# Kernel tuning notes

Hardware: AMD Instinct MI355X
Metric: run time of the kernel (lower is better)

## Reference

```python
import jax, jax.numpy as jnp
import numpy as np

NUM_TRUE = 8
NUM_NULL = 2
NUM_EXPERTS = NUM_TRUE + NUM_NULL
TOP_K = 2


def setup_inputs() -> dict:
    key = jax.random.key(0)
    k0, k1, k2 = jax.random.split(key, 3)
    B, S, D = 4, 2048, 1024
    inputs = jax.random.normal(k0, (B, S, D), dtype=jnp.float32)
    gate_w = jax.random.normal(k1, (NUM_EXPERTS, D), dtype=jnp.float32) * 0.02
    gate_b = jnp.zeros((NUM_EXPERTS,), dtype=jnp.float32)
    # expert_w stored as [E, D_in, D_out] so expert i computes x @ expert_w[i] + expert_b[i]
    expert_w = jax.random.normal(k2, (NUM_TRUE, D, D), dtype=jnp.float32) * 0.02
    expert_b = jnp.zeros((NUM_TRUE, D), dtype=jnp.float32)
    return {"inputs": inputs, "gate_w": gate_w, "gate_b": gate_b,
            "expert_w": expert_w, "expert_b": expert_b}


def reference(inputs, gate_w, gate_b, expert_w, expert_b):
    D = inputs.shape[-1]
    x = inputs.reshape(-1, D)                       # [T, D]
    gate_logits = x @ gate_w.T + gate_b             # [T, E]
    gate_probs = jax.nn.softmax(gate_logits, axis=-1)
    weights, selected = jax.lax.top_k(gate_probs, TOP_K)  # [T, K]
    true_mask = selected < NUM_TRUE                 # null experts contribute nothing
    true_weights = weights * true_mask
    denom = true_weights.sum(axis=-1, keepdims=True)
    denom = jnp.where(denom > 0, denom, jnp.ones_like(denom))
    norm_w = (true_weights / denom).astype(x.dtype)  # [T, K]
    # per-(token, true-expert) combine weight; zero for unselected experts
    one_hot = jax.nn.one_hot(selected, NUM_EXPERTS, dtype=norm_w.dtype)  # [T, K, E]
    combine_w = jnp.einsum('tk,tke->te', norm_w, one_hot)[:, :NUM_TRUE]  # [T, E_true]
    # dense expert evaluation, then weighted combine (zero weights cancel
    # exactly as the gather/scatter loop in the torch code)
    expert_out = jnp.einsum('td,edh->teh', x, expert_w) + expert_b[None, :, :]  # [T, E_true, D]
    out = jnp.einsum('te,teh->th', combine_w, expert_out)  # [T, D]
    return out.reshape(inputs.shape[:-1] + (out.shape[-1],))
```

## Files before the change

kernel.cpp:

```cpp
#include <hip/hip_runtime.h>
#include <hip/hip_bf16.h>
#include <stdint.h>

#define T_TOKENS 8192
#define D_DIM    1024
#define NE       10
#define NT       8

typedef unsigned short u16;
typedef __attribute__((ext_vector_type(8))) __bf16 bf16x8;
typedef __attribute__((ext_vector_type(4))) float  f32x4;

__device__ __forceinline__ u16 f32_to_bf16(float f) {
  union { float f; uint32_t u; } v; v.f = f;
  uint32_t u = v.u;
  return (u16)((u + 0x7fffu + ((u >> 16) & 1u)) >> 16);
}

__device__ __forceinline__ void async_load16(const u16* g, u16* l) {
  __builtin_amdgcn_global_load_lds(
      (const __attribute__((address_space(1))) void*)(const void*)g,
      (__attribute__((address_space(3))) void*)(void*)l, 16, 0, 0);
}

__global__ __launch_bounds__(256) void gate_kernel(
    const float* __restrict__ x, const float* __restrict__ gw,
    const float* __restrict__ gb, u16* __restrict__ xb,
    int* __restrict__ cnt, int* __restrict__ tokList, float* __restrict__ wList) {
  __shared__ float gws[NE * D_DIM];
  __shared__ float gbs[NE];
  __shared__ int   se[32];
  __shared__ float swt[32];
  int tid = threadIdx.x;
  for (int i = tid; i < NE * D_DIM; i += 256) gws[i] = gw[i];
  if (tid < NE) gbs[tid] = gb[tid];
  __syncthreads();
  int lane = tid & 63;
  int wv   = tid >> 6;
  for (int it = 0; it < 4; ++it) {
    int slot = wv * 4 + it;
    int t = blockIdx.x * 16 + slot;
    const float* xr = x + (size_t)t * D_DIM;
    float xv[16];
#pragma unroll
    for (int j = 0; j < 16; ++j) xv[j] = xr[lane + 64 * j];
#pragma unroll
    for (int j = 0; j < 16; ++j)
      xb[(size_t)t * D_DIM + lane + 64 * j] = f32_to_bf16(xv[j]);
    float logit[NE];
#pragma unroll
    for (int e = 0; e < NE; ++e) {
      float a = 0.f;
#pragma unroll
      for (int j = 0; j < 16; ++j)
        a = fmaf(xv[j], gws[e * D_DIM + lane + 64 * j], a);
#pragma unroll
      for (int off = 32; off >= 1; off >>= 1) a += __shfl_xor(a, off);
      logit[e] = a + gbs[e];
    }
    float mx = logit[0];
#pragma unroll
    for (int e = 1; e < NE; ++e) mx = fmaxf(mx, logit[e]);
    float p[NE]; float s = 0.f;
#pragma unroll
    for (int e = 0; e < NE; ++e) { p[e] = expf(logit[e] - mx); s += p[e]; }
    int e0 = 0; float b0 = p[0];
#pragma unroll
    for (int e = 1; e < NE; ++e) if (p[e] > b0) { b0 = p[e]; e0 = e; }
    int e1 = -1; float b1 = -1.f;
#pragma unroll
    for (int e = 0; e < NE; ++e) if (e != e0 && p[e] > b1) { b1 = p[e]; e1 = e; }
    float w0 = b0 / s, w1 = b1 / s;
    float tw0 = (e0 < NT) ? w0 : 0.f;
    float tw1 = (e1 < NT) ? w1 : 0.f;
    float denom = tw0 + tw1;
    float nw0 = 0.f, nw1 = 0.f;
    if (denom > 0.f) { nw0 = tw0 / denom; nw1 = tw1 / denom; }
    if (lane == 0) {
      se[slot * 2]      = (e0 < NT) ? e0 : -1;  swt[slot * 2]      = nw0;
      se[slot * 2 + 1]  = (e1 < NT) ? e1 : -1;  swt[slot * 2 + 1]  = nw1;
    }
  }
  __syncthreads();
  if (tid < NT * 2) {
    int e = tid >> 1, sl = tid & 1, c = 0;
    for (int i = sl; i < 32; i += 2) c += (se[i] == e);
    if (c > 0) {
      int seg = e * 2 + sl;
      int base = atomicAdd(&cnt[seg * 32], c);
      int j = 0;
      for (int i = sl; i < 32; i += 2) {
        if (se[i] == e) {
          tokList[seg * T_TOKENS + base + j] = blockIdx.x * 16 + (i >> 1);
          wList[seg * T_TOKENS + base + j]   = swt[i];
          ++j;
        }
      }
    }
  }
}

__global__ __launch_bounds__(256) void transpose_w(
    const float* __restrict__ W, u16* __restrict__ wT) {
  __shared__ float tile[64][65];
  int e  = blockIdx.z;
  int k0 = blockIdx.y * 64;
  int n0 = blockIdx.x * 64;
  int c  = threadIdx.x & 63;
  int r0 = threadIdx.x >> 6;
  const float* We = W + ((size_t)e << 20);
#pragma unroll
  for (int rr = 0; rr < 16; ++rr) {
    int r = rr * 4 + r0;
    tile[c][r] = We[(size_t)(k0 + r) * 1024 + n0 + c];
  }
  __syncthreads();
  u16* wTe = wT + ((size_t)e << 20);
#pragma unroll
  for (int rr = 0; rr < 16; ++rr) {
    int n = rr * 4 + r0;
    wTe[(size_t)(n0 + n) * 1024 + k0 + c] = f32_to_bf16(tile[n][c]);
  }
}

__global__ __launch_bounds__(256) void moe_gemm(
    const u16* __restrict__ xb, const u16* __restrict__ wT,
    const int* __restrict__ cnt, const int* __restrict__ tokList,
    const float* __restrict__ wList, const float* __restrict__ eb,
    float* __restrict__ out, int slot, int accum) {
  int e   = blockIdx.z;
  int seg = e * 2 + slot;
  int c   = cnt[seg * 32];
  int m0  = blockIdx.y * 128;
  if (m0 >= c) return;
  int n0  = blockIdx.x * 128;
  __shared__ __align__(16) u16 As[128 * 32];
  __shared__ __align__(16) u16 Bs[128 * 32];
  __shared__ int   tokS[128];
  __shared__ float wS[128];
  int tid = threadIdx.x;
  if (tid < 128) {
    int gm = m0 + tid;
    bool v = gm < c;
    tokS[tid] = v ? tokList[seg * T_TOKENS + gm] : 0;
    wS[tid]   = v ? wList[seg * T_TOKENS + gm]  : 0.f;
  }
  __syncthreads();
  int lane = tid & 63;
  int wv   = tid >> 6;
  int rl   = lane >> 2;
  int kcp  = lane & 3;
  int kcd  = kcp ^ (rl & 3);
  int rowL0 = wv * 32 + rl, rowL1 = rowL0 + 16;
  const u16* gA0 = xb + (size_t)tokS[rowL0] * 1024 + kcd * 8;
  const u16* gA1 = xb + (size_t)tokS[rowL1] * 1024 + kcd * 8;
  const u16* wTe = wT + ((size_t)e << 20);
  const u16* gB0 = wTe + (size_t)(n0 + rowL0) * 1024 + kcd * 8;
  const u16* gB1 = wTe + (size_t)(n0 + rowL1) * 1024 + kcd * 8;
  u16* lA0 = As + (wv * 32) * 32;
  u16* lA1 = As + (wv * 32 + 16) * 32;
  u16* lB0 = Bs + (wv * 32) * 32;
  u16* lB1 = Bs + (wv * 32 + 16) * 32;

  int wm = wv >> 1, wn = wv & 1;
  int lrow = lane & 15;
  int q    = lane >> 4;
  int sw   = (q ^ (lrow & 3)) * 8;
  f32x4 acc[4][4];
#pragma unroll
  for (int i = 0; i < 4; ++i)
#pragma unroll
    for (int j = 0; j < 4; ++j) acc[i][j] = (f32x4){0.f, 0.f, 0.f, 0.f};

  for (int k0 = 0; k0 < 1024; k0 += 32) {
    __syncthreads();
    async_load16(gA0 + k0, lA0);
    async_load16(gA1 + k0, lA1);
    async_load16(gB0 + k0, lB0);
    async_load16(gB1 + k0, lB1);
    __syncthreads();
    bf16x8 af[4], bfr[4];
#pragma unroll
    for (int mt = 0; mt < 4; ++mt)
      af[mt] = *(const bf16x8*)(As + (wm * 64 + mt * 16 + lrow) * 32 + sw);
#pragma unroll
    for (int nt = 0; nt < 4; ++nt)
      bfr[nt] = *(const bf16x8*)(Bs + (wn * 64 + nt * 16 + lrow) * 32 + sw);
#pragma unroll
    for (int mt = 0; mt < 4; ++mt)
#pragma unroll
      for (int nt = 0; nt < 4; ++nt)
        acc[mt][nt] = __builtin_amdgcn_mfma_f32_16x16x32_bf16(
            af[mt], bfr[nt], acc[mt][nt], 0, 0, 0);
  }
  int rq = lane >> 4;
  float bias[4];
#pragma unroll
  for (int nt = 0; nt < 4; ++nt)
    bias[nt] = eb[e * 1024 + n0 + wn * 64 + nt * 16 + lrow];
#pragma unroll
  for (int mt = 0; mt < 4; ++mt) {
#pragma unroll
    for (int r = 0; r < 4; ++r) {
      int ml = wm * 64 + mt * 16 + rq * 4 + r;
      if (m0 + ml < c) {
        int   t = tokS[ml];
        float w = wS[ml];
        float* orow = out + (size_t)t * 1024 + n0 + wn * 64 + lrow;
        if (accum) {
#pragma unroll
          for (int nt = 0; nt < 4; ++nt)
            orow[nt * 16] += w * (acc[mt][nt][r] + bias[nt]);
        } else {
#pragma unroll
          for (int nt = 0; nt < 4; ++nt)
            orow[nt * 16] = w * (acc[mt][nt][r] + bias[nt]);
        }
      }
    }
  }
}

extern "C" void kernel_launch(void* const* d_in, const int* in_sizes, int n_in,
                              void* d_out, int out_size, void* d_ws, size_t ws_size,
                              hipStream_t stream) {
  const float* x  = (const float*)d_in[0];
  const float* gw = (const float*)d_in[1];
  const float* gb = (const float*)d_in[2];
  const float* ew = (const float*)d_in[3];
  const float* eb = (const float*)d_in[4];
  float* out = (float*)d_out;
  char* ws = (char*)d_ws;
  int*   cnt     = (int*)ws;
  int*   tokList = (int*)(ws + 2048);
  float* wList   = (float*)(ws + 2048 + 16 * T_TOKENS * 4);
  u16*   xb      = (u16*)(ws + 2048 + 2 * 16 * T_TOKENS * 4);
  u16*   wT      = (u16*)(ws + 2048 + 2 * 16 * T_TOKENS * 4 + (size_t)T_TOKENS * D_DIM * 2);

  hipMemsetAsync(cnt, 0, 2048, stream);
  hipMemsetAsync(d_out, 0, (size_t)out_size * sizeof(float), stream);
  gate_kernel<<<512, 256, 0, stream>>>(x, gw, gb, xb, cnt, tokList, wList);
  transpose_w<<<dim3(16, 16, 8), 256, 0, stream>>>(ew, wT);
  moe_gemm<<<dim3(8, 24, 8), 256, 0, stream>>>(xb, wT, cnt, tokList, wList, eb, out, 0, 0);
  moe_gemm<<<dim3(8, 24, 8), 256, 0, stream>>>(xb, wT, cnt, tokList, wList, eb, out, 1, 1);
}
```

Baseline: 212.2 us.

## Merge MoE GEMM slots per expert, write bf16 outputs, add gather combine kernel

```diff
diff --git a/kernel.cpp b/kernel.cpp
--- a/kernel.cpp
+++ b/kernel.cpp
@@ -6,18 +6,24 @@
 #define D_DIM    1024
 #define NE       10
 #define NT       8
+#define SEG      2048
 
 typedef unsigned short u16;
 typedef __attribute__((ext_vector_type(8))) __bf16 bf16x8;
 typedef __attribute__((ext_vector_type(4))) float  f32x4;
-
-__device__ __forceinline__ u16 f32_to_bf16(float f) {
+typedef __attribute__((ext_vector_type(8))) unsigned short u16x8;
+typedef __attribute__((ext_vector_type(4))) unsigned short u16x4;
+
+static __device__ __forceinline__ u16 f32_to_bf16(float f) {
   union { float f; uint32_t u; } v; v.f = f;
   uint32_t u = v.u;
   return (u16)((u + 0x7fffu + ((u >> 16) & 1u)) >> 16);
 }
-
-__device__ __forceinline__ void async_load16(const u16* g, u16* l) {
+static __device__ __forceinline__ float bf16_to_f32(u16 u) {
+  union { uint32_t u; float f; } v; v.u = ((uint32_t)u) << 16; return v.f;
+}
+
+static __device__ __forceinline__ void async_load16(const u16* g, u16* l) {
   __builtin_amdgcn_global_load_lds(
       (const __attribute__((address_space(1))) void*)(const void*)g,
       (__attribute__((address_space(3))) void*)(void*)l, 16, 0, 0);
@@ -26,34 +32,48 @@
 __global__ __launch_bounds__(256) void gate_kernel(
     const float* __restrict__ x, const float* __restrict__ gw,
     const float* __restrict__ gb, u16* __restrict__ xb,
-    int* __restrict__ cnt, int* __restrict__ tokList, float* __restrict__ wList) {
+    int* __restrict__ cnt, int* __restrict__ tokList,
+    int* __restrict__ revIdx, float* __restrict__ revW) {
   __shared__ float gws[NE * D_DIM];
   __shared__ float gbs[NE];
   __shared__ int   se[32];
   __shared__ float swt[32];
   int tid = threadIdx.x;
-  for (int i = tid; i < NE * D_DIM; i += 256) gws[i] = gw[i];
+  {
+    const f32x4* g4 = (const f32x4*)gw;
+    f32x4* s4 = (f32x4*)gws;
+    for (int i = tid; i < NE * D_DIM / 4; i += 256) s4[i] = g4[i];
+  }
   if (tid < NE) gbs[tid] = gb[tid];
   __syncthreads();
   int lane = tid & 63;
   int wv   = tid >> 6;
+  const f32x4* gws4 = (const f32x4*)gws;
   for (int it = 0; it < 4; ++it) {
     int slot = wv * 4 + it;
     int t = blockIdx.x * 16 + slot;
-    const float* xr = x + (size_t)t * D_DIM;
-    float xv[16];
-#pragma unroll
-    for (int j = 0; j < 16; ++j) xv[j] = xr[lane + 64 * j];
-#pragma unroll
-    for (int j = 0; j < 16; ++j)
-      xb[(size_t)t * D_DIM + lane + 64 * j] = f32_to_bf16(xv[j]);
+    const f32x4* xr4 = (const f32x4*)(x + (size_t)t * D_DIM);
+    f32x4 xv[4];
+#pragma unroll
+    for (int jj = 0; jj < 4; ++jj) xv[jj] = xr4[lane + 64 * jj];
+    u16x4* xbr = (u16x4*)(xb + (size_t)t * D_DIM);
+#pragma unroll
+    for (int jj = 0; jj < 4; ++jj) {
+      u16x4 pk;
+#pragma unroll
+      for (int k = 0; k < 4; ++k) pk[k] = f32_to_bf16(xv[jj][k]);
+      xbr[lane + 64 * jj] = pk;
+    }
     float logit[NE];
 #pragma unroll
     for (int e = 0; e < NE; ++e) {
       float a = 0.f;
 #pragma unroll
-      for (int j = 0; j < 16; ++j)
-        a = fmaf(xv[j], gws[e * D_DIM + lane + 64 * j], a);
+      for (int jj = 0; jj < 4; ++jj) {
+        f32x4 gv = gws4[e * 256 + lane + 64 * jj];
+#pragma unroll
+        for (int k = 0; k < 4; ++k) a = fmaf(xv[jj][k], gv[k], a);
+      }
 #pragma unroll
       for (int off = 32; off >= 1; off >>= 1) a += __shfl_xor(a, off);
       logit[e] = a + gbs[e];
@@ -77,22 +97,26 @@
     float nw0 = 0.f, nw1 = 0.f;
     if (denom > 0.f) { nw0 = tw0 / denom; nw1 = tw1 / denom; }
     if (lane == 0) {
-      se[slot * 2]      = (e0 < NT) ? e0 : -1;  swt[slot * 2]      = nw0;
-      se[slot * 2 + 1]  = (e1 < NT) ? e1 : -1;  swt[slot * 2 + 1]  = nw1;
+      se[slot * 2]     = (e0 < NT) ? e0 : -1;  swt[slot * 2]     = nw0;
+      se[slot * 2 + 1] = (e1 < NT) ? e1 : -1;  swt[slot * 2 + 1] = nw1;
+      if (e0 >= NT) { revIdx[t * 2]     = -1; revW[t * 2]     = 0.f; }
+      if (e1 >= NT) { revIdx[t * 2 + 1] = -1; revW[t * 2 + 1] = 0.f; }
     }
   }
   __syncthreads();
-  if (tid < NT * 2) {
-    int e = tid >> 1, sl = tid & 1, c = 0;
-    for (int i = sl; i < 32; i += 2) c += (se[i] == e);
+  if (tid < NT) {
+    int e = tid, c = 0;
+    for (int i = 0; i < 32; ++i) c += (se[i] == e);
     if (c > 0) {
-      int seg = e * 2 + sl;
-      int base = atomicAdd(&cnt[seg * 32], c);
+      int base = atomicAdd(&cnt[e * 32], c);
       int j = 0;
-      for (int i = sl; i < 32; i += 2) {
+      for (int i = 0; i < 32; ++i) {
         if (se[i] == e) {
-          tokList[seg * T_TOKENS + base + j] = blockIdx.x * 16 + (i >> 1);
-          wList[seg * T_TOKENS + base + j]   = swt[i];
+          int tt  = blockIdx.x * 16 + (i >> 1);
+          int pos = base + j;
+          tokList[e * SEG + pos]   = tt;
+          revIdx[tt * 2 + (i & 1)] = e * SEG + pos;
+          revW[tt * 2 + (i & 1)]   = swt[i];
           ++j;
         }
       }
@@ -126,41 +150,32 @@
 __global__ __launch_bounds__(256) void moe_gemm(
     const u16* __restrict__ xb, const u16* __restrict__ wT,
     const int* __restrict__ cnt, const int* __restrict__ tokList,
-    const float* __restrict__ wList, const float* __restrict__ eb,
-    float* __restrict__ out, int slot, int accum) {
-  int e   = blockIdx.z;
-  int seg = e * 2 + slot;
-  int c   = cnt[seg * 32];
-  int m0  = blockIdx.y * 128;
+    const float* __restrict__ eb, u16* __restrict__ ybuf) {
+  int e  = blockIdx.x;
+  int c  = cnt[e * 32];
+  int m0 = blockIdx.z * 128;
   if (m0 >= c) return;
-  int n0  = blockIdx.x * 128;
-  __shared__ __align__(16) u16 As[128 * 32];
-  __shared__ __align__(16) u16 Bs[128 * 32];
-  __shared__ int   tokS[128];
-  __shared__ float wS[128];
+  int n0 = blockIdx.y * 128;
+  __shared__ __align__(16) u16 As[2][128 * 32];
+  __shared__ __align__(16) u16 Bs[2][128 * 32];
+  __shared__ int tokS[128];
   int tid = threadIdx.x;
   if (tid < 128) {
     int gm = m0 + tid;
-    bool v = gm < c;
-    tokS[tid] = v ? tokList[seg * T_TOKENS + gm] : 0;
-    wS[tid]   = v ? wList[seg * T_TOKENS + gm]  : 0.f;
+    tokS[tid] = (gm < c) ? tokList[e * SEG + gm] : tokList[e * SEG];
   }
   __syncthreads();
   int lane = tid & 63;
   int wv   = tid >> 6;
-  int rl   = lane >> 2;
-  int kcp  = lane & 3;
-  int kcd  = kcp ^ (rl & 3);
+  int rl  = lane >> 2;
+  int kcp = lane & 3;
+  int kcd = kcp ^ (rl & 3);
   int rowL0 = wv * 32 + rl, rowL1 = rowL0 + 16;
   const u16* gA0 = xb + (size_t)tokS[rowL0] * 1024 + kcd * 8;
   const u16* gA1 = xb + (size_t)tokS[rowL1] * 1024 + kcd * 8;
   const u16* wTe = wT + ((size_t)e << 20);
   const u16* gB0 = wTe + (size_t)(n0 + rowL0) * 1024 + kcd * 8;
   const u16* gB1 = wTe + (size_t)(n0 + rowL1) * 1024 + kcd * 8;
-  u16* lA0 = As + (wv * 32) * 32;
-  u16* lA1 = As + (wv * 32 + 16) * 32;
-  u16* lB0 = Bs + (wv * 32) * 32;
-  u16* lB1 = Bs + (wv * 32 + 16) * 32;
 
   int wm = wv >> 1, wn = wv & 1;
   int lrow = lane & 15;
@@ -172,20 +187,32 @@
 #pragma unroll
     for (int j = 0; j < 4; ++j) acc[i][j] = (f32x4){0.f, 0.f, 0.f, 0.f};
 
-  for (int k0 = 0; k0 < 1024; k0 += 32) {
-    __syncthreads();
-    async_load16(gA0 + k0, lA0);
-    async_load16(gA1 + k0, lA1);
-    async_load16(gB0 + k0, lB0);
-    async_load16(gB1 + k0, lB1);
-    __syncthreads();
+  async_load16(gA0, As[0] + (wv * 32) * 32);
+  async_load16(gA1, As[0] + (wv * 32 + 16) * 32);
+  async_load16(gB0, Bs[0] + (wv * 32) * 32);
+  async_load16(gB1, Bs[0] + (wv * 32 + 16) * 32);
+
+  for (int kt = 0; kt < 32; ++kt) {
+    int cur = kt & 1;
+    if (kt < 31) {
+      asm volatile("s_barrier" ::: "memory");
+      int ko = (kt + 1) * 32;
+      async_load16(gA0 + ko, As[1 - cur] + (wv * 32) * 32);
+      async_load16(gA1 + ko, As[1 - cur] + (wv * 32 + 16) * 32);
+      async_load16(gB0 + ko, Bs[1 - cur] + (wv * 32) * 32);
+      async_load16(gB1 + ko, Bs[1 - cur] + (wv * 32 + 16) * 32);
+      asm volatile("s_waitcnt vmcnt(4)" ::: "memory");
+    } else {
+      asm volatile("s_waitcnt vmcnt(0)" ::: "memory");
+    }
+    asm volatile("s_barrier" ::: "memory");
     bf16x8 af[4], bfr[4];
 #pragma unroll
     for (int mt = 0; mt < 4; ++mt)
-      af[mt] = *(const bf16x8*)(As + (wm * 64 + mt * 16 + lrow) * 32 + sw);
+      af[mt] = *(const bf16x8*)(As[cur] + (wm * 64 + mt * 16 + lrow) * 32 + sw);
 #pragma unroll
     for (int nt = 0; nt < 4; ++nt)
-      bfr[nt] = *(const bf16x8*)(Bs + (wn * 64 + nt * 16 + lrow) * 32 + sw);
+      bfr[nt] = *(const bf16x8*)(Bs[cur] + (wn * 64 + nt * 16 + lrow) * 32 + sw);
 #pragma unroll
     for (int mt = 0; mt < 4; ++mt)
 #pragma unroll
@@ -198,26 +225,58 @@
 #pragma unroll
   for (int nt = 0; nt < 4; ++nt)
     bias[nt] = eb[e * 1024 + n0 + wn * 64 + nt * 16 + lrow];
+  u16* yb = ybuf + ((size_t)(e * SEG + m0)) * 1024 + n0 + wn * 64 + lrow;
 #pragma unroll
   for (int mt = 0; mt < 4; ++mt) {
 #pragma unroll
     for (int r = 0; r < 4; ++r) {
       int ml = wm * 64 + mt * 16 + rq * 4 + r;
-      if (m0 + ml < c) {
-        int   t = tokS[ml];
-        float w = wS[ml];
-        float* orow = out + (size_t)t * 1024 + n0 + wn * 64 + lrow;
-        if (accum) {
-#pragma unroll
-          for (int nt = 0; nt < 4; ++nt)
-            orow[nt * 16] += w * (acc[mt][nt][r] + bias[nt]);
-        } else {
-#pragma unroll
-          for (int nt = 0; nt < 4; ++nt)
-            orow[nt * 16] = w * (acc[mt][nt][r] + bias[nt]);
-        }
-      }
-    }
+      u16* row = yb + (size_t)ml * 1024;
+#pragma unroll
+      for (int nt = 0; nt < 4; ++nt)
+        row[nt * 16] = f32_to_bf16(acc[mt][nt][r] + bias[nt]);
+    }
+  }
+}
+
+__global__ __launch_bounds__(256) void combine_kernel(
+    const u16* __restrict__ ybuf, const int* __restrict__ revIdx,
+    const float* __restrict__ revW, float* __restrict__ out) {
+  int tid = threadIdx.x, lane = tid & 63, wv = tid >> 6;
+  for (int it = 0; it < 4; ++it) {
+    int t  = blockIdx.x * 16 + wv * 4 + it;
+    int i0 = revIdx[t * 2], i1 = revIdx[t * 2 + 1];
+    float w0 = revW[t * 2], w1 = revW[t * 2 + 1];
+    float o[16];
+#pragma unroll
+    for (int k = 0; k < 16; ++k) o[k] = 0.f;
+    if (i0 >= 0) {
+      const u16x8* y = (const u16x8*)(ybuf + (size_t)i0 * 1024);
+#pragma unroll
+      for (int jj = 0; jj < 2; ++jj) {
+        u16x8 v = y[lane + 64 * jj];
+#pragma unroll
+        for (int k = 0; k < 8; ++k) o[jj * 8 + k] += w0 * bf16_to_f32(v[k]);
+      }
+    }
+    if (i1 >= 0) {
+      const u16x8* y = (const u16x8*)(ybuf + (size_t)i1 * 1024);
+#pragma unroll
+      for (int jj = 0; jj < 2; ++jj) {
+        u16x8 v = y[lane + 64 * jj];
+#pragma unroll
+        for (int k = 0; k < 8; ++k) o[jj * 8 + k] += w1 * bf16_to_f32(v[k]);
+      }
+    }
+    f32x4* o4 = (f32x4*)(out + (size_t)t * 1024);
+#pragma unroll
+    for (int jj = 0; jj < 2; ++jj)
+#pragma unroll
+      for (int h = 0; h < 2; ++h) {
+        f32x4 vv = {o[jj * 8 + h * 4], o[jj * 8 + h * 4 + 1],
+                    o[jj * 8 + h * 4 + 2], o[jj * 8 + h * 4 + 3]};
+        o4[2 * (lane + 64 * jj) + h] = vv;
+      }
   }
 }
 
@@ -232,15 +291,16 @@
   float* out = (float*)d_out;
   char* ws = (char*)d_ws;
   int*   cnt     = (int*)ws;
-  int*   tokList = (int*)(ws + 2048);
-  float* wList   = (float*)(ws + 2048 + 16 * T_TOKENS * 4);
-  u16*   xb      = (u16*)(ws + 2048 + 2 * 16 * T_TOKENS * 4);
-  u16*   wT      = (u16*)(ws + 2048 + 2 * 16 * T_TOKENS * 4 + (size_t)T_TOKENS * D_DIM * 2);
-
-  hipMemsetAsync(cnt, 0, 2048, stream);
-  hipMemsetAsync(d_out, 0, (size_t)out_size * sizeof(float), stream);
-  gate_kernel<<<512, 256, 0, stream>>>(x, gw, gb, xb, cnt, tokList, wList);
+  int*   tokList = (int*)(ws + 4096);
+  int*   revIdx  = (int*)(ws + 4096 + 65536);
+  float* revW    = (float*)(ws + 4096 + 131072);
+  u16*   xb      = (u16*)(ws + 200704);
+  u16*   wT      = (u16*)(ws + 200704 + 16777216);
+  u16*   ybuf    = (u16*)(ws + 200704 + 33554432);
+
+  hipMemsetAsync(cnt, 0, 4096, stream);
+  gate_kernel<<<512, 256, 0, stream>>>(x, gw, gb, xb, cnt, tokList, revIdx, revW);
   transpose_w<<<dim3(16, 16, 8), 256, 0, stream>>>(ew, wT);
-  moe_gemm<<<dim3(8, 24, 8), 256, 0, stream>>>(xb, wT, cnt, tokList, wList, eb, out, 0, 0);
-  moe_gemm<<<dim3(8, 24, 8), 256, 0, stream>>>(xb, wT, cnt, tokList, wList, eb, out, 1, 1);
-}
+  moe_gemm<<<dim3(8, 8, 16), 256, 0, stream>>>(xb, wT, cnt, tokList, eb, ybuf);
+  combine_kernel<<<512, 256, 0, stream>>>(ybuf, revIdx, revW, out);
+}
```

Measured after the change: 188.0 us. -11.4%, faster.
